# Kernel optimization log

Hardware: AMD Instinct MI355X
Metric: run time of the kernel (lower is better)

The kernel has to match this reference:

```python
import jax, jax.numpy as jnp
import numpy as np

B, DIN, DOUT, Q, H1, H2 = 4096, 768, 512, 64, 32, 64
EPS = 1e-5

def setup_inputs() -> dict:
    key = jax.random.key(0)
    ks = jax.random.split(key, 12)
    s = lambda fan_in: 1.0 / np.sqrt(fan_in)
    return {
        "x": jax.random.normal(ks[0], (B, DIN), jnp.float32),
        # proj_in: Linear(dim_in, dim_out)
        "wp": jax.random.uniform(ks[1], (DIN, DOUT), jnp.float32, -s(DIN), s(DIN)),
        "bp": jax.random.uniform(ks[2], (DOUT,), jnp.float32, -s(DIN), s(DIN)),
        # inner: Linear(1, H1) -> ReLU -> Linear(H1, Q)
        "wi1": jax.random.uniform(ks[3], (H1,), jnp.float32, -1.0, 1.0),
        "bi1": jax.random.uniform(ks[4], (H1,), jnp.float32, -1.0, 1.0),
        "wi2": jax.random.uniform(ks[5], (H1, Q), jnp.float32, -s(H1), s(H1)),
        "bi2": jax.random.uniform(ks[6], (Q,), jnp.float32, -s(H1), s(H1)),
        # outer: Linear(1, H2) -> ReLU -> Linear(H2, dim_out)
        "wo1": jax.random.uniform(ks[7], (H2,), jnp.float32, -1.0, 1.0),
        "bo1": jax.random.uniform(ks[8], (H2,), jnp.float32, -1.0, 1.0),
        "wo2": jax.random.uniform(ks[9], (H2, DOUT), jnp.float32, -s(H2), s(H2)),
        "bo2": jax.random.uniform(ks[10], (DOUT,), jnp.float32, -s(H2), s(H2)),
        # LayerNorm(dim_out)
        "gamma": jnp.ones((DOUT,), jnp.float32),
        "beta": jnp.zeros((DOUT,), jnp.float32),
    }

def _per_scalar_mlp(v, w1, b1, w2, b2):
    # v: [...] scalars -> tiny MLP 1->h->out applied per scalar -> [..., out]
    h = jax.nn.relu(v[..., None] * w1 + b1)          # [..., h]
    return jnp.einsum("...h,ho->...o", h, w2) + b2   # [..., out]

def reference(x, wp, bp, wi1, bi1, wi2, bi2, wo1, bo1, wo2, bo2, gamma, beta):
    x_proj = x @ wp + bp                                    # [B, DOUT]
    inner_out = _per_scalar_mlp(x_proj, wi1, bi1, wi2, bi2)  # [B, DOUT, Q]
    u = inner_out.sum(axis=1)                               # [B, Q]
    outer_out = _per_scalar_mlp(u, wo1, bo1, wo2, bo2)      # [B, Q, DOUT]
    summed = outer_out.sum(axis=1)                          # [B, DOUT]
    mu = summed.mean(axis=-1, keepdims=True)
    var = jnp.var(summed, axis=-1, keepdims=True)
    return (summed - mu) * jax.lax.rsqrt(var + EPS) * gamma + beta
```

## Files before the change

### kernel.cpp

```cpp
#include <hip/hip_runtime.h>
#include <hip/hip_bf16.h>

#define B_ROWS 4096
#define DIN    768
#define DOUT   512
#define QDIM   64
#define H1C    32
#define H2C    64

#define W_BP    0
#define W_WI1   512
#define W_BI1   544
#define W_WI2   576
#define W_BI2   2624
#define W_WO1   2688
#define W_BO1   2752
#define W_WO2   2816
#define W_BO2   35584
#define W_GAM   36096
#define W_BET   36608
#define W_TOT   37120

typedef short  short8_t  __attribute__((ext_vector_type(8)));
typedef __bf16 bf16x8_t  __attribute__((ext_vector_type(8)));
typedef float  f32x4_t   __attribute__((ext_vector_type(4)));

__device__ __forceinline__ float bf16bits_to_f32(unsigned short u) {
  return __builtin_bit_cast(float, ((unsigned int)u) << 16);
}
__device__ __forceinline__ unsigned short f32_to_bf16bits(float f) {
  return __builtin_bit_cast(unsigned short, __float2bfloat16(f));
}
__device__ __forceinline__ float ldf(const void* p, int i, bool isb) {
  if (isb) return bf16bits_to_f32(((const unsigned short*)p)[i]);
  return ((const float*)p)[i];
}
__device__ __forceinline__ bool detect_bf16(const unsigned int* xw, int t) {
  const unsigned int w = xw[t & 63];
  const unsigned int e = (w >> 7) & 0xffu;
  const bool hit = (e >= 118u && e <= 127u);
  return __popcll(__ballot(hit)) >= 40;
}

__global__ __launch_bounds__(256) void k_prep(
    const void* __restrict__ x, const void* __restrict__ wp,
    const void* __restrict__ bp,
    const void* __restrict__ wi1, const void* __restrict__ bi1,
    const void* __restrict__ wi2, const void* __restrict__ bi2,
    const void* __restrict__ wo1, const void* __restrict__ bo1,
    const void* __restrict__ wo2, const void* __restrict__ bo2,
    const void* __restrict__ gamma, const void* __restrict__ beta,
    unsigned short* __restrict__ xb,
    unsigned short* __restrict__ wpT,
    float* __restrict__ wW)
{
  const int t = threadIdx.x, b = blockIdx.x;
  const bool isb = detect_bf16((const unsigned int*)x, t);

  if (b < 384) {
    const int base = b * 8192 + t * 4;
#pragma unroll
    for (int j = 0; j < 8; ++j) {
      const int idx = base + j * 1024;
      if (isb) {
        *(uint2*)&xb[idx] = *(const uint2*)((const unsigned short*)x + idx);
      } else {
        const float4 f = *(const float4*)((const float*)x + idx);
        ushort4 o;
        o.x = f32_to_bf16bits(f.x); o.y = f32_to_bf16bits(f.y);
        o.z = f32_to_bf16bits(f.z); o.w = f32_to_bf16bits(f.w);
        *(ushort4*)&xb[idx] = o;
      }
    }
  } else if (b < 768) {
    __shared__ unsigned short tile[32][33];
    const int tb = b - 384;
    const int n0 = (tb & 15) * 32, k0 = (tb >> 4) * 32;
    const int tx = t & 31, ty = t >> 5;
#pragma unroll
    for (int i = 0; i < 32; i += 8)
      tile[ty + i][tx] = f32_to_bf16bits(ldf(wp, (k0 + ty + i) * DOUT + n0 + tx, isb));
    __syncthreads();
#pragma unroll
    for (int i = 0; i < 32; i += 8)
      wpT[(size_t)(n0 + ty + i) * DIN + k0 + tx] = tile[tx][ty + i];
  } else {
    for (int e = (b - 768) * 256 + t; e < W_TOT; e += 8 * 256) {
      float v;
      if      (e < W_WI1) v = ldf(bp,    e - W_BP,  isb);
      else if (e < W_BI1) v = ldf(wi1,   e - W_WI1, isb);
      else if (e < W_WI2) v = ldf(bi1,   e - W_BI1, isb);
      else if (e < W_BI2) v = ldf(wi2,   e - W_WI2, isb);
      else if (e < W_WO1) v = ldf(bi2,   e - W_BI2, isb);
      else if (e < W_BO1) v = ldf(wo1,   e - W_WO1, isb);
      else if (e < W_WO2) v = ldf(bo1,   e - W_BO1, isb);
      else if (e < W_BO2) v = ldf(wo2,   e - W_WO2, isb);
      else if (e < W_GAM) v = ldf(bo2,   e - W_BO2, isb);
      else if (e < W_BET) v = ldf(gamma, e - W_GAM, isb);
      else                v = ldf(beta,  e - W_BET, isb);
      wW[e] = v;
    }
  }
}

__global__ __launch_bounds__(512, 2) void k_main(
    const unsigned int* __restrict__ xw,
    const unsigned short* __restrict__ xb,
    const unsigned short* __restrict__ wpT,
    const float* __restrict__ wW,
    void* __restrict__ out)
{
  __shared__ alignas(16) char smem[44416];
  unsigned short* As   = (unsigned short*)smem;
  float* sXp   = (float*)smem;
  float* sS    = (float*)(smem + 33024);
  float* sU    = (float*)(smem + 35072);
  float* sT    = (float*)(smem + 39168);
  float* sRed  = (float*)(smem + 43264);
  float* sStats= (float*)(smem + 44288);

  const int t    = threadIdx.x;
  const int wv   = t >> 6, lane = t & 63;
  const int lm   = lane & 15, quad = lane >> 4;
  const int b0   = blockIdx.x * 16;
  const bool isb = detect_bf16(xw, t);

  for (int e = t; e < 16 * 96; e += 512) {
    const int r = e / 96, c = (e % 96) * 8;
    *(short8_t*)&As[r * 776 + c] =
        *(const short8_t*)(xb + (size_t)(b0 + r) * DIN + c);
  }
  __syncthreads();

  f32x4_t acc[4] = {};
  const unsigned short* wb0 = wpT + (size_t)(wv * 64 + lm) * DIN + quad * 8;
  short8_t bcur[4], bnxt[4];
#pragma unroll
  for (int nt = 0; nt < 4; ++nt)
    bcur[nt] = *(const short8_t*)(wb0 + nt * 16 * DIN);
  for (int kt = 0; kt < 24; ++kt) {
    const int kn = (kt < 23) ? kt + 1 : 23;
#pragma unroll
    for (int nt = 0; nt < 4; ++nt)
      bnxt[nt] = *(const short8_t*)(wb0 + nt * 16 * DIN + kn * 32);
    const short8_t av = *(const short8_t*)&As[lm * 776 + kt * 32 + quad * 8];
    const bf16x8_t af = __builtin_bit_cast(bf16x8_t, av);
#pragma unroll
    for (int nt = 0; nt < 4; ++nt)
      acc[nt] = __builtin_amdgcn_mfma_f32_16x16x32_bf16(
          af, __builtin_bit_cast(bf16x8_t, bcur[nt]), acc[nt], 0, 0, 0);
#pragma unroll
    for (int nt = 0; nt < 4; ++nt) bcur[nt] = bnxt[nt];
  }
  __syncthreads();

#pragma unroll
  for (int nt = 0; nt < 4; ++nt) {
    const int col = wv * 64 + nt * 16 + lm;
    const float bpv = wW[W_BP + col];
#pragma unroll
    for (int i = 0; i < 4; ++i)
      sXp[(quad * 4 + i) * 516 + col] = acc[nt][i] + bpv;
  }
  __syncthreads();

  {
    const int h = t & 31, r = t >> 5;
    const float w = wW[W_WI1 + h], bb = wW[W_BI1 + h];
    const float* row = &sXp[r * 516];
    float a = 0.f;
    for (int d = 0; d < 512; d += 4) {
      const float4 v = *(const float4*)&row[d];
      a += fmaxf(fmaf(v.x, w, bb), 0.f);
      a += fmaxf(fmaf(v.y, w, bb), 0.f);
      a += fmaxf(fmaf(v.z, w, bb), 0.f);
      a += fmaxf(fmaf(v.w, w, bb), 0.f);
    }
    sS[r * H1C + h] = a;
  }
  __syncthreads();

  for (int e = t; e < 16 * QDIM; e += 512) {
    const int r = e >> 6, q = e & 63;
    float a = 0.f;
#pragma unroll
    for (int h = 0; h < H1C; ++h)
      a = fmaf(sS[r * H1C + h], wW[W_WI2 + h * QDIM + q], a);
    sU[e] = a + 512.f * wW[W_BI2 + q];
  }
  __syncthreads();

  for (int e = t; e < 16 * H2C; e += 512) {
    const int r = e >> 6, g = e & 63;
    const float w = wW[W_WO1 + g], bb = wW[W_BO1 + g];
    float a = 0.f;
#pragma unroll
    for (int q = 0; q < QDIM; ++q)
      a += fmaxf(fmaf(sU[r * QDIM + q], w, bb), 0.f);
    sT[e] = a;
  }
  __syncthreads();

  const int d0 = t;
  float a[16];
#pragma unroll
  for (int r = 0; r < 16; ++r) a[r] = 0.f;
  for (int g = 0; g < H2C; ++g) {
    const float w = wW[W_WO2 + g * DOUT + d0];
#pragma unroll
    for (int r = 0; r < 16; ++r)
      a[r] = fmaf(sT[r * H2C + g], w, a[r]);
  }
  const float bo2v = 64.f * wW[W_BO2 + d0];
#pragma unroll
  for (int r = 0; r < 16; ++r) a[r] += bo2v;

  float pr[16], prs[16];
#pragma unroll
  for (int r = 0; r < 16; ++r) { pr[r] = a[r]; prs[r] = a[r] * a[r]; }
#pragma unroll
  for (int off = 1; off < 64; off <<= 1) {
#pragma unroll
    for (int r = 0; r < 16; ++r) {
      pr[r]  += __shfl_xor(pr[r],  off);
      prs[r] += __shfl_xor(prs[r], off);
    }
  }
  if (lane == 0) {
#pragma unroll
    for (int r = 0; r < 16; ++r) {
      sRed[(wv * 16 + r) * 2 + 0] = pr[r];
      sRed[(wv * 16 + r) * 2 + 1] = prs[r];
    }
  }
  __syncthreads();
  if (t < 16) {
    float sm = 0.f, sq = 0.f;
#pragma unroll
    for (int w = 0; w < 8; ++w) {
      sm += sRed[(w * 16 + t) * 2 + 0];
      sq += sRed[(w * 16 + t) * 2 + 1];
    }
    const float mu  = sm * (1.f / 512.f);
    const float var = fmaxf(sq * (1.f / 512.f) - mu * mu, 0.f);
    sStats[t * 2 + 0] = mu;
    sStats[t * 2 + 1] = rsqrtf(var + 1e-5f);
  }
  __syncthreads();

  const float gm = wW[W_GAM + d0], bt = wW[W_BET + d0];
#pragma unroll
  for (int r = 0; r < 16; ++r) {
    const float o = (a[r] - sStats[r * 2 + 0]) * sStats[r * 2 + 1] * gm + bt;
    if (isb)
      ((unsigned short*)out)[(size_t)(b0 + r) * DOUT + d0] = f32_to_bf16bits(o);
    else
      ((float*)out)[(size_t)(b0 + r) * DOUT + d0] = o;
  }
}

extern "C" void kernel_launch(void* const* d_in, const int* in_sizes, int n_in,
                              void* d_out, int out_size, void* d_ws, size_t ws_size,
                              hipStream_t stream) {
  const void* x     = d_in[0];
  const void* wp    = d_in[1];

  char* ws = (char*)d_ws;
  unsigned short* xb  = (unsigned short*)ws;
  unsigned short* wpT = (unsigned short*)(ws + 6291456);
  float*          wW  = (float*)(ws + 7077888);

  k_prep<<<776, 256, 0, stream>>>(x, wp, d_in[2], d_in[3], d_in[4], d_in[5],
                                  d_in[6], d_in[7], d_in[8], d_in[9], d_in[10],
                                  d_in[11], d_in[12], xb, wpT, wW);
  k_main<<<B_ROWS / 16, 512, 0, stream>>>((const unsigned int*)x, xb, wpT, wW, d_out);
}
```

Baseline: 134.5 us.

## Fuse x conversion into main kernel, use MFMA for outer projection, 1024 threads

Drops the separate x-to-bf16 pass from the prep kernel and converts x tiles while loading them into shared memory in the main kernel, which removes a full write and re-read of the activations. The outer Linear(H2, DOUT) now runs as bf16 MFMA against a pre-transposed wo2, replacing the scalar FMA loop. The block grows to 1024 threads, so each wave computes fewer output columns, and the inner ReLU sum is split across lanes with shuffle reductions. In exchange, the second GEMM is rounded to bf16 and occupancy drops to a single large block per CU slot.

```diff
diff --git a/kernel.cpp b/kernel.cpp
--- a/kernel.cpp
+++ b/kernel.cpp
@@ -21,6 +21,10 @@
 #define W_BET   36608
 #define W_TOT   37120
 
+#define WS_WPT  0
+#define WS_WO2T 786432
+#define WS_WW   851968
+
 typedef short  short8_t  __attribute__((ext_vector_type(8)));
 typedef __bf16 bf16x8_t  __attribute__((ext_vector_type(8)));
 typedef float  f32x4_t   __attribute__((ext_vector_type(4)));
@@ -50,33 +54,17 @@
     const void* __restrict__ wo1, const void* __restrict__ bo1,
     const void* __restrict__ wo2, const void* __restrict__ bo2,
     const void* __restrict__ gamma, const void* __restrict__ beta,
-    unsigned short* __restrict__ xb,
     unsigned short* __restrict__ wpT,
+    unsigned short* __restrict__ wo2T,
     float* __restrict__ wW)
 {
   const int t = threadIdx.x, b = blockIdx.x;
   const bool isb = detect_bf16((const unsigned int*)x, t);
+  const int tx = t & 31, ty = t >> 5;
 
   if (b < 384) {
-    const int base = b * 8192 + t * 4;
-#pragma unroll
-    for (int j = 0; j < 8; ++j) {
-      const int idx = base + j * 1024;
-      if (isb) {
-        *(uint2*)&xb[idx] = *(const uint2*)((const unsigned short*)x + idx);
-      } else {
-        const float4 f = *(const float4*)((const float*)x + idx);
-        ushort4 o;
-        o.x = f32_to_bf16bits(f.x); o.y = f32_to_bf16bits(f.y);
-        o.z = f32_to_bf16bits(f.z); o.w = f32_to_bf16bits(f.w);
-        *(ushort4*)&xb[idx] = o;
-      }
-    }
-  } else if (b < 768) {
     __shared__ unsigned short tile[32][33];
-    const int tb = b - 384;
-    const int n0 = (tb & 15) * 32, k0 = (tb >> 4) * 32;
-    const int tx = t & 31, ty = t >> 5;
+    const int n0 = (b & 15) * 32, k0 = (b >> 4) * 32;
 #pragma unroll
     for (int i = 0; i < 32; i += 8)
       tile[ty + i][tx] = f32_to_bf16bits(ldf(wp, (k0 + ty + i) * DOUT + n0 + tx, isb));
@@ -84,8 +72,19 @@
 #pragma unroll
     for (int i = 0; i < 32; i += 8)
       wpT[(size_t)(n0 + ty + i) * DIN + k0 + tx] = tile[tx][ty + i];
+  } else if (b < 416) {
+    __shared__ unsigned short tile[32][33];
+    const int tb = b - 384;
+    const int c0 = (tb & 15) * 32, g0 = (tb >> 4) * 32;
+#pragma unroll
+    for (int i = 0; i < 32; i += 8)
+      tile[ty + i][tx] = f32_to_bf16bits(ldf(wo2, (g0 + ty + i) * DOUT + c0 + tx, isb));
+    __syncthreads();
+#pragma unroll
+    for (int i = 0; i < 32; i += 8)
+      wo2T[(size_t)(c0 + ty + i) * QDIM + g0 + tx] = tile[tx][ty + i];
   } else {
-    for (int e = (b - 768) * 256 + t; e < W_TOT; e += 8 * 256) {
+    for (int e = (b - 416) * 256 + t; e < W_TOT; e += 8 * 256) {
       float v;
       if      (e < W_WI1) v = ldf(bp,    e - W_BP,  isb);
       else if (e < W_BI1) v = ldf(wi1,   e - W_WI1, isb);
@@ -103,175 +102,227 @@
   }
 }
 
-__global__ __launch_bounds__(512, 2) void k_main(
-    const unsigned int* __restrict__ xw,
-    const unsigned short* __restrict__ xb,
+__global__ __launch_bounds__(1024) void k_main(
+    const void* __restrict__ x,
     const unsigned short* __restrict__ wpT,
+    const unsigned short* __restrict__ wo2T,
     const float* __restrict__ wW,
     void* __restrict__ out)
 {
-  __shared__ alignas(16) char smem[44416];
+  __shared__ alignas(16) char smem[43904];
   unsigned short* As   = (unsigned short*)smem;
-  float* sXp   = (float*)smem;
-  float* sS    = (float*)(smem + 33024);
-  float* sU    = (float*)(smem + 35072);
-  float* sT    = (float*)(smem + 39168);
-  float* sRed  = (float*)(smem + 43264);
-  float* sStats= (float*)(smem + 44288);
+  float*          sXp  = (float*)smem;
+  float*          sS   = (float*)(smem + 33024);
+  float*          sU   = (float*)(smem + 35072);
+  unsigned short* sTb  = (unsigned short*)(smem + 39168);
+  float*          sRed = (float*)(smem + 41472);
+  float*          sSt  = (float*)(smem + 43520);
+  float*          sW1  = (float*)(smem + 43648);
+  float*          sB1  = (float*)(smem + 43776);
 
   const int t    = threadIdx.x;
   const int wv   = t >> 6, lane = t & 63;
   const int lm   = lane & 15, quad = lane >> 4;
   const int b0   = blockIdx.x * 16;
-  const bool isb = detect_bf16(xw, t);
-
-  for (int e = t; e < 16 * 96; e += 512) {
-    const int r = e / 96, c = (e % 96) * 8;
-    *(short8_t*)&As[r * 776 + c] =
-        *(const short8_t*)(xb + (size_t)(b0 + r) * DIN + c);
-  }
-  __syncthreads();
-
-  f32x4_t acc[4] = {};
-  const unsigned short* wb0 = wpT + (size_t)(wv * 64 + lm) * DIN + quad * 8;
-  short8_t bcur[4], bnxt[4];
-#pragma unroll
-  for (int nt = 0; nt < 4; ++nt)
-    bcur[nt] = *(const short8_t*)(wb0 + nt * 16 * DIN);
+  const bool isb = detect_bf16((const unsigned int*)x, t);
+
+#pragma unroll
+  for (int i = 0; i < 3; ++i) {
+    const int c = i * 1024 + t;
+    const int row = c / 192, off = (c - row * 192) * 4;
+    unsigned short a4[4];
+    if (isb) {
+      const uint2 v = *(const uint2*)((const unsigned short*)x + (size_t)(b0 + row) * DIN + off);
+      *(uint2*)a4 = v;
+    } else {
+      const float4 f = *(const float4*)((const float*)x + (size_t)(b0 + row) * DIN + off);
+      a4[0] = f32_to_bf16bits(f.x); a4[1] = f32_to_bf16bits(f.y);
+      a4[2] = f32_to_bf16bits(f.z); a4[3] = f32_to_bf16bits(f.w);
+    }
+    *(uint2*)&As[row * 776 + off] = *(const uint2*)a4;
+  }
+  if (t < 32) { sW1[t] = wW[W_WI1 + t]; sB1[t] = wW[W_BI1 + t]; }
+
+  const unsigned short* wb0 = wpT + (size_t)(wv * 32 + lm) * DIN + quad * 8;
+  const unsigned short* wb1 = wb0 + 16 * DIN;
+  short8_t c0 = *(const short8_t*)wb0;
+  short8_t c1 = *(const short8_t*)wb1;
+  short8_t n0 = *(const short8_t*)(wb0 + 32);
+  short8_t n1 = *(const short8_t*)(wb1 + 32);
+  __syncthreads();
+
+  f32x4_t acc0 = {}, acc1 = {};
+#pragma unroll
   for (int kt = 0; kt < 24; ++kt) {
-    const int kn = (kt < 23) ? kt + 1 : 23;
-#pragma unroll
-    for (int nt = 0; nt < 4; ++nt)
-      bnxt[nt] = *(const short8_t*)(wb0 + nt * 16 * DIN + kn * 32);
+    const short8_t f0 = *(const short8_t*)(wb0 + (kt + 2) * 32);
+    const short8_t f1 = *(const short8_t*)(wb1 + (kt + 2) * 32);
     const short8_t av = *(const short8_t*)&As[lm * 776 + kt * 32 + quad * 8];
     const bf16x8_t af = __builtin_bit_cast(bf16x8_t, av);
-#pragma unroll
-    for (int nt = 0; nt < 4; ++nt)
-      acc[nt] = __builtin_amdgcn_mfma_f32_16x16x32_bf16(
-          af, __builtin_bit_cast(bf16x8_t, bcur[nt]), acc[nt], 0, 0, 0);
-#pragma unroll
-    for (int nt = 0; nt < 4; ++nt) bcur[nt] = bnxt[nt];
-  }
-  __syncthreads();
-
-#pragma unroll
-  for (int nt = 0; nt < 4; ++nt) {
-    const int col = wv * 64 + nt * 16 + lm;
-    const float bpv = wW[W_BP + col];
-#pragma unroll
-    for (int i = 0; i < 4; ++i)
-      sXp[(quad * 4 + i) * 516 + col] = acc[nt][i] + bpv;
-  }
-  __syncthreads();
-
-  {
-    const int h = t & 31, r = t >> 5;
-    const float w = wW[W_WI1 + h], bb = wW[W_BI1 + h];
-    const float* row = &sXp[r * 516];
+    acc0 = __builtin_amdgcn_mfma_f32_16x16x32_bf16(af, __builtin_bit_cast(bf16x8_t, c0), acc0, 0, 0, 0);
+    acc1 = __builtin_amdgcn_mfma_f32_16x16x32_bf16(af, __builtin_bit_cast(bf16x8_t, c1), acc1, 0, 0, 0);
+    c0 = n0; c1 = n1; n0 = f0; n1 = f1;
+  }
+  __syncthreads();
+
+  {
+    const int ca = wv * 32 + lm, cb = ca + 16;
+    const float bpa = wW[W_BP + ca], bpb = wW[W_BP + cb];
+#pragma unroll
+    for (int i = 0; i < 4; ++i) {
+      sXp[(quad * 4 + i) * 516 + ca] = acc0[i] + bpa;
+      sXp[(quad * 4 + i) * 516 + cb] = acc1[i] + bpb;
+    }
+  }
+  __syncthreads();
+
+  {
+    const int r = wv, cg = lane & 31, hg = lane >> 5;
+    const float* row = &sXp[r * 516 + cg * 16];
+    float xc[16];
+#pragma unroll
+    for (int j = 0; j < 4; ++j) {
+      const float4 v = *(const float4*)&row[j * 4];
+      xc[j*4+0] = v.x; xc[j*4+1] = v.y; xc[j*4+2] = v.z; xc[j*4+3] = v.w;
+    }
+    float S16[16];
+#pragma unroll
+    for (int j = 0; j < 16; ++j) {
+      const float w = sW1[hg * 16 + j], bb = sB1[hg * 16 + j];
+      float a = 0.f;
+#pragma unroll
+      for (int c = 0; c < 16; ++c) a += fmaxf(fmaf(xc[c], w, bb), 0.f);
+      S16[j] = a;
+    }
+#pragma unroll
+    for (int off = 1; off < 32; off <<= 1)
+#pragma unroll
+      for (int j = 0; j < 16; ++j) S16[j] += __shfl_xor(S16[j], off);
+    if (cg == 0) {
+#pragma unroll
+      for (int j = 0; j < 16; ++j) sS[r * 32 + hg * 16 + j] = S16[j];
+    }
+  }
+  __syncthreads();
+
+  {
+    const int r = t >> 6, q = t & 63;
     float a = 0.f;
-    for (int d = 0; d < 512; d += 4) {
-      const float4 v = *(const float4*)&row[d];
+#pragma unroll
+    for (int h4 = 0; h4 < 32; h4 += 4) {
+      const float4 s4 = *(const float4*)&sS[r * 32 + h4];
+      a = fmaf(s4.x, wW[W_WI2 + (h4 + 0) * QDIM + q], a);
+      a = fmaf(s4.y, wW[W_WI2 + (h4 + 1) * QDIM + q], a);
+      a = fmaf(s4.z, wW[W_WI2 + (h4 + 2) * QDIM + q], a);
+      a = fmaf(s4.w, wW[W_WI2 + (h4 + 3) * QDIM + q], a);
+    }
+    sU[t] = a + 512.f * wW[W_BI2 + q];
+  }
+  __syncthreads();
+
+  {
+    const int r = t >> 6, g = t & 63;
+    const float w = wW[W_WO1 + g], bb = wW[W_BO1 + g];
+    float a = 0.f;
+#pragma unroll
+    for (int q = 0; q < QDIM; q += 4) {
+      const float4 v = *(const float4*)&sU[r * 64 + q];
       a += fmaxf(fmaf(v.x, w, bb), 0.f);
       a += fmaxf(fmaf(v.y, w, bb), 0.f);
       a += fmaxf(fmaf(v.z, w, bb), 0.f);
       a += fmaxf(fmaf(v.w, w, bb), 0.f);
     }
-    sS[r * H1C + h] = a;
-  }
-  __syncthreads();
-
-  for (int e = t; e < 16 * QDIM; e += 512) {
-    const int r = e >> 6, q = e & 63;
-    float a = 0.f;
-#pragma unroll
-    for (int h = 0; h < H1C; ++h)
-      a = fmaf(sS[r * H1C + h], wW[W_WI2 + h * QDIM + q], a);
-    sU[e] = a + 512.f * wW[W_BI2 + q];
-  }
-  __syncthreads();
-
-  for (int e = t; e < 16 * H2C; e += 512) {
-    const int r = e >> 6, g = e & 63;
-    const float w = wW[W_WO1 + g], bb = wW[W_BO1 + g];
-    float a = 0.f;
-#pragma unroll
-    for (int q = 0; q < QDIM; ++q)
-      a += fmaxf(fmaf(sU[r * QDIM + q], w, bb), 0.f);
-    sT[e] = a;
-  }
-  __syncthreads();
-
-  const int d0 = t;
-  float a[16];
-#pragma unroll
-  for (int r = 0; r < 16; ++r) a[r] = 0.f;
-  for (int g = 0; g < H2C; ++g) {
-    const float w = wW[W_WO2 + g * DOUT + d0];
-#pragma unroll
-    for (int r = 0; r < 16; ++r)
-      a[r] = fmaf(sT[r * H2C + g], w, a[r]);
-  }
-  const float bo2v = 64.f * wW[W_BO2 + d0];
-#pragma unroll
-  for (int r = 0; r < 16; ++r) a[r] += bo2v;
-
-  float pr[16], prs[16];
-#pragma unroll
-  for (int r = 0; r < 16; ++r) { pr[r] = a[r]; prs[r] = a[r] * a[r]; }
-#pragma unroll
-  for (int off = 1; off < 64; off <<= 1) {
-#pragma unroll
-    for (int r = 0; r < 16; ++r) {
-      pr[r]  += __shfl_xor(pr[r],  off);
-      prs[r] += __shfl_xor(prs[r], off);
-    }
-  }
-  if (lane == 0) {
-#pragma unroll
-    for (int r = 0; r < 16; ++r) {
-      sRed[(wv * 16 + r) * 2 + 0] = pr[r];
-      sRed[(wv * 16 + r) * 2 + 1] = prs[r];
+    sTb[r * 72 + g] = f32_to_bf16bits(a);
+  }
+  __syncthreads();
+
+  f32x4_t sa0 = {}, sa1 = {};
+  {
+    const unsigned short* wcol0 = wo2T + (size_t)(wv * 32 + lm) * QDIM + quad * 8;
+    const unsigned short* wcol1 = wcol0 + 16 * QDIM;
+#pragma unroll
+    for (int kt = 0; kt < 2; ++kt) {
+      const short8_t aT = *(const short8_t*)&sTb[lm * 72 + kt * 32 + quad * 8];
+      const bf16x8_t aTf = __builtin_bit_cast(bf16x8_t, aT);
+      const short8_t bW0 = *(const short8_t*)(wcol0 + kt * 32);
+      const short8_t bW1 = *(const short8_t*)(wcol1 + kt * 32);
+      sa0 = __builtin_amdgcn_mfma_f32_16x16x32_bf16(aTf, __builtin_bit_cast(bf16x8_t, bW0), sa0, 0, 0, 0);
+      sa1 = __builtin_amdgcn_mfma_f32_16x16x32_bf16(aTf, __builtin_bit_cast(bf16x8_t, bW1), sa1, 0, 0, 0);
+    }
+  }
+  const int colA = wv * 32 + lm, colB = colA + 16;
+  {
+    const float bzA = 64.f * wW[W_BO2 + colA];
+    const float bzB = 64.f * wW[W_BO2 + colB];
+#pragma unroll
+    for (int i = 0; i < 4; ++i) { sa0[i] += bzA; sa1[i] += bzB; }
+  }
+  {
+    float pr[4], prs[4];
+#pragma unroll
+    for (int i = 0; i < 4; ++i) {
+      pr[i]  = sa0[i] + sa1[i];
+      prs[i] = sa0[i] * sa0[i] + sa1[i] * sa1[i];
+    }
+#pragma unroll
+    for (int off = 1; off < 16; off <<= 1)
+#pragma unroll
+      for (int i = 0; i < 4; ++i) {
+        pr[i]  += __shfl_xor(pr[i],  off);
+        prs[i] += __shfl_xor(prs[i], off);
+      }
+    if (lm == 0) {
+#pragma unroll
+      for (int i = 0; i < 4; ++i) {
+        sRed[(wv * 16 + quad * 4 + i) * 2 + 0] = pr[i];
+        sRed[(wv * 16 + quad * 4 + i) * 2 + 1] = prs[i];
+      }
     }
   }
   __syncthreads();
   if (t < 16) {
     float sm = 0.f, sq = 0.f;
 #pragma unroll
-    for (int w = 0; w < 8; ++w) {
+    for (int w = 0; w < 16; ++w) {
       sm += sRed[(w * 16 + t) * 2 + 0];
       sq += sRed[(w * 16 + t) * 2 + 1];
     }
     const float mu  = sm * (1.f / 512.f);
     const float var = fmaxf(sq * (1.f / 512.f) - mu * mu, 0.f);
-    sStats[t * 2 + 0] = mu;
-    sStats[t * 2 + 1] = rsqrtf(var + 1e-5f);
-  }
-  __syncthreads();
-
-  const float gm = wW[W_GAM + d0], bt = wW[W_BET + d0];
-#pragma unroll
-  for (int r = 0; r < 16; ++r) {
-    const float o = (a[r] - sStats[r * 2 + 0]) * sStats[r * 2 + 1] * gm + bt;
-    if (isb)
-      ((unsigned short*)out)[(size_t)(b0 + r) * DOUT + d0] = f32_to_bf16bits(o);
-    else
-      ((float*)out)[(size_t)(b0 + r) * DOUT + d0] = o;
+    sSt[t * 2 + 0] = mu;
+    sSt[t * 2 + 1] = rsqrtf(var + 1e-5f);
+  }
+  __syncthreads();
+
+  {
+    const float gA = wW[W_GAM + colA], bA = wW[W_BET + colA];
+    const float gB = wW[W_GAM + colB], bB = wW[W_BET + colB];
+#pragma unroll
+    for (int i = 0; i < 4; ++i) {
+      const int r = quad * 4 + i;
+      const float mu = sSt[r * 2 + 0], rstd = sSt[r * 2 + 1];
+      const float oA = (sa0[i] - mu) * rstd * gA + bA;
+      const float oB = (sa1[i] - mu) * rstd * gB + bB;
+      if (isb) {
+        ((unsigned short*)out)[(size_t)(b0 + r) * DOUT + colA] = f32_to_bf16bits(oA);
+        ((unsigned short*)out)[(size_t)(b0 + r) * DOUT + colB] = f32_to_bf16bits(oB);
+      } else {
+        ((float*)out)[(size_t)(b0 + r) * DOUT + colA] = oA;
+        ((float*)out)[(size_t)(b0 + r) * DOUT + colB] = oB;
+      }
+    }
   }
 }
 
 extern "C" void kernel_launch(void* const* d_in, const int* in_sizes, int n_in,
                               void* d_out, int out_size, void* d_ws, size_t ws_size,
                               hipStream_t stream) {
-  const void* x     = d_in[0];
-  const void* wp    = d_in[1];
-
   char* ws = (char*)d_ws;
-  unsigned short* xb  = (unsigned short*)ws;
-  unsigned short* wpT = (unsigned short*)(ws + 6291456);
-  float*          wW  = (float*)(ws + 7077888);
-
-  k_prep<<<776, 256, 0, stream>>>(x, wp, d_in[2], d_in[3], d_in[4], d_in[5],
-                                  d_in[6], d_in[7], d_in[8], d_in[9], d_in[10],
-                                  d_in[11], d_in[12], xb, wpT, wW);
-  k_main<<<B_ROWS / 16, 512, 0, stream>>>((const unsigned int*)x, xb, wpT, wW, d_out);
-}
+  unsigned short* wpT  = (unsigned short*)(ws + WS_WPT);
+  unsigned short* wo2T = (unsigned short*)(ws + WS_WO2T);
+  float*          wW   = (float*)(ws + WS_WW);
+
+  k_prep<<<424, 256, 0, stream>>>(d_in[0], d_in[1], d_in[2], d_in[3], d_in[4],
+                                  d_in[5], d_in[6], d_in[7], d_in[8], d_in[9],
+                                  d_in[10], d_in[11], d_in[12], wpT, wo2T, wW);
+  k_main<<<B_ROWS / 16, 1024, 0, stream>>>(d_in[0], wpT, wo2T, wW, d_out);
+}
```

Result: no change. 136.6 us (+1.5%).
